# Kernel tuning notes

Measured on AMD Instinct MI355X. Metric: run time of the kernel, lower is better.

The kernel has to match this reference:

```python
import jax, jax.numpy as jnp
import numpy as np

B, C, D, H, W = 2, 96, 32, 64, 64
K = 2            # MRConv stride
EPS = 1e-5
SLOPE = 0.2      # LeakyReLU negative slope used by ViG act_layer('leakyrelu')


def conv1x1(x, w, b):
    # 1x1x1 Conv3d == per-voxel channel GEMM. x: [B,Ci,D,H,W], w: [Co,Ci]
    return jnp.einsum('bcdhw,oc->bodhw', x, w) + b[None, :, None, None, None]


def batchnorm(x, g, b):
    # training-mode BatchNorm3d: stats over (B, D, H, W)
    m = x.mean(axis=(0, 2, 3, 4), keepdims=True)
    v = x.var(axis=(0, 2, 3, 4), keepdims=True)
    return (x - m) * jax.lax.rsqrt(v + EPS) * g[None, :, None, None, None] + b[None, :, None, None, None]


def instnorm(x, g, b):
    # InstanceNorm3d: stats over (D, H, W) per sample/channel
    m = x.mean(axis=(2, 3, 4), keepdims=True)
    v = x.var(axis=(2, 3, 4), keepdims=True)
    return (x - m) * jax.lax.rsqrt(v + EPS) * g[None, :, None, None, None] + b[None, :, None, None, None]


def lrelu(x):
    return jnp.where(x >= 0, x, SLOPE * x)


def mr_aggregate(x):
    # MRConv shift/subtract/max, in closed form.
    # Original: x_j = max over axes a, shifts s in range(K, L_a, K) of (x - roll(x, s, a)), init 0.
    # Since shifts cover ALL nonzero multiples of K mod L_a (L_a % K == 0), the rolled values at a
    # position are exactly the other members of its residue class mod K along that axis, and
    # max(0, x - min_excluding_self) == x - min_including_self.  Hence:
    #   x_j = x - min over axes of (strided residue-class min along that axis).
    def axmin(x, axis):
        L = x.shape[axis]
        shp = list(x.shape)
        grp = shp[:axis] + [L // K, K] + shp[axis + 1:]
        xg = x.reshape(grp)
        m = xg.min(axis=axis, keepdims=True)             # min over same residue class
        return jnp.broadcast_to(m, grp).reshape(shp)
    m = jnp.minimum(jnp.minimum(axmin(x, 2), axmin(x, 3)), axmin(x, 4))
    return x - m


def setup_inputs() -> dict:
    key = jax.random.key(0)
    ks = jax.random.split(key, 8)
    f32 = jnp.float32
    def w(k, co, ci):
        return (jax.random.normal(k, (co, ci), dtype=f32) / np.sqrt(ci)).astype(f32)
    return {
        'x': jax.random.normal(ks[0], (B, C, D, H, W), dtype=f32),
        'w_fc1': w(ks[1], C, C), 'b_fc1': jnp.zeros((C,), f32),
        'g_bn1': jnp.ones((C,), f32), 'be_bn1': jnp.zeros((C,), f32),
        'w_g': w(ks[2], 2 * C, 2 * C), 'b_g': jnp.zeros((2 * C,), f32),
        'g_in': jnp.ones((2 * C,), f32), 'be_in': jnp.zeros((2 * C,), f32),
        'w_fc2': w(ks[3], C, 2 * C), 'b_fc2': jnp.zeros((C,), f32),
        'g_bn2': jnp.ones((C,), f32), 'be_bn2': jnp.zeros((C,), f32),
        'w_f1': w(ks[4], 4 * C, C), 'b_f1': jnp.zeros((4 * C,), f32),
        'g_bnf1': jnp.ones((4 * C,), f32), 'be_bnf1': jnp.zeros((4 * C,), f32),
        'w_f2': w(ks[5], C, 4 * C), 'b_f2': jnp.zeros((C,), f32),
        'g_bnf2': jnp.ones((C,), f32), 'be_bnf2': jnp.zeros((C,), f32),
    }


def reference(x, w_fc1, b_fc1, g_bn1, be_bn1, w_g, b_g, g_in, be_in,
              w_fc2, b_fc2, g_bn2, be_bn2, w_f1, b_f1, g_bnf1, be_bnf1,
              w_f2, b_f2, g_bnf2, be_bnf2):
    # ---- Grapher ----
    shortcut = x
    h = batchnorm(conv1x1(x, w_fc1, b_fc1), g_bn1, be_bn1)          # fc1: Conv+BN
    xj = mr_aggregate(h)                                            # MRConv shift-max agg
    hc = jnp.concatenate([h, xj], axis=1)                           # [B,2C,D,H,W]
    hg = lrelu(instnorm(conv1x1(hc, w_g, b_g), g_in, be_in))        # BasicConv: Conv+IN+LeakyReLU
    h = batchnorm(conv1x1(hg, w_fc2, b_fc2), g_bn2, be_bn2)         # fc2: Conv+BN
    x = h + shortcut
    # ---- FFN ----
    shortcut = x
    h = batchnorm(conv1x1(x, w_f1, b_f1), g_bnf1, be_bnf1)
    h = lrelu(h)
    h = batchnorm(conv1x1(h, w_f2, b_f2), g_bnf2, be_bnf2)
    return h + shortcut
```

## Files before the change

### kernel.cpp

```cpp
#include <hip/hip_runtime.h>
#include <hip/hip_bf16.h>


typedef __hip_bfloat16 bf16;
typedef __attribute__((ext_vector_type(8))) short short8;
typedef __attribute__((ext_vector_type(4))) float f4;
typedef __attribute__((ext_vector_type(4))) unsigned short us4;

#define DEV static __device__ __forceinline__

constexpr int Sq  = 131072;
constexpr int NVq = 262144;

DEV float bu2f(unsigned short u) { return __uint_as_float(((unsigned)u) << 16); }
DEV unsigned short f2bu(float f) {
    unsigned i = __float_as_uint(f);
    unsigned r = i + 0x7FFFu + ((i >> 16) & 1u);
    return (unsigned short)(r >> 16);
}
DEV void glds16(const void* g, void* l) {
    __builtin_amdgcn_global_load_lds(
        (const __attribute__((address_space(1))) unsigned*)g,
        (__attribute__((address_space(3))) unsigned*)l, 16, 0, 0);
}

template<int CIRB, int KP, int CO, int BN, int AMODE, bool PERB>
__global__ __launch_bounds__(256)
void conv_k(const char* __restrict__ A0, const char* __restrict__ A1,
            const char* __restrict__ Wb, const float* __restrict__ bias,
            const float* __restrict__ cfA, const float* __restrict__ cfB,
            bf16* __restrict__ Y, float* __restrict__ part)
{
    constexpr int NSTEP = KP / 64;
    constexpr int NF = BN / 16;
    constexpr int BI = BN / 8;
    __shared__ __align__(16) char smem[16384 + BN * 128];
    char* As = smem;
    char* Bs = smem + 16384;

    const int tid = threadIdx.x;
    const int lane = tid & 63, wid = tid >> 6, l16 = lane & 15, lhi = lane >> 4;
    const int gm = blockIdx.x, gy = blockIdx.y;
    const int v0 = gm * 128;
    const int b = gm >> 10;
    const int n0g = gy * BN;

    f4 acc[2][NF];
#pragma unroll
    for (int nf = 0; nf < NF; ++nf) {
        float bb = bias[n0g + nf * 16 + l16];
        f4 t = {bb, bb, bb, bb};
        acc[0][nf] = t; acc[1][nf] = t;
    }

    for (int s = 0; s < NSTEP; ++s) {
        for (int i = wid; i < BI; i += 4) {
            int o = i * 8 + (lane >> 3);
            glds16(Wb + (size_t)(n0g + o) * (KP * 2) + s * 128 + (((lane & 7) ^ (o & 7)) << 4),
                   Bs + i * 1024);
        }
        if constexpr (AMODE == 0) {
            for (int i = wid; i < 16; i += 4) {
                int r = i * 8 + (lane >> 3);
                glds16(A0 + (size_t)(v0 + r) * CIRB + s * 128 + (((lane & 7) ^ (r & 7)) << 4),
                       As + i * 1024);
            }
        } else {
#pragma unroll
            for (int j = 0; j < 4; ++j) {
                int idx = tid + 256 * j;
                int v = idx >> 3, u = idx & 7;
                int k8 = s * 8 + u;
                short8 hh;
                if constexpr (AMODE == 2) {
                    short8 raw = *(const short8*)(A0 + (size_t)(v0 + v) * CIRB + k8 * 16);
                    int cb = b * KP + k8 * 8;
                    f4 a0 = *(const f4*)(cfA + cb), a1 = *(const f4*)(cfA + cb + 4);
                    f4 d0 = *(const f4*)(cfB + cb), d1 = *(const f4*)(cfB + cb + 4);
#pragma unroll
                    for (int e = 0; e < 4; ++e) {
                        float t0 = fmaf(a0[e], bu2f((unsigned short)raw[e]),     d0[e]);
                        float t1 = fmaf(a1[e], bu2f((unsigned short)raw[e + 4]), d1[e]);
                        t0 = fmaxf(t0, 0.2f * t0);
                        t1 = fmaxf(t1, 0.2f * t1);
                        hh[e] = (short)f2bu(t0); hh[e + 4] = (short)f2bu(t1);
                    }
                } else {
                    if (k8 < 12) {
                        short8 raw = *(const short8*)(A0 + (size_t)(v0 + v) * 192 + k8 * 16);
                        int cb = k8 * 8;
                        f4 a0 = *(const f4*)(cfA + cb), a1 = *(const f4*)(cfA + cb + 4);
                        f4 d0 = *(const f4*)(cfB + cb), d1 = *(const f4*)(cfB + cb + 4);
#pragma unroll
                        for (int e = 0; e < 4; ++e) {
                            hh[e]     = (short)f2bu(fmaf(a0[e], bu2f((unsigned short)raw[e]),     d0[e]));
                            hh[e + 4] = (short)f2bu(fmaf(a1[e], bu2f((unsigned short)raw[e + 4]), d1[e]));
                        }
                    } else {
                        hh = *(const short8*)(A1 + (size_t)(v0 + v) * 192 + (k8 - 12) * 16);
                    }
                }
                *(short8*)(As + v * 128 + ((u ^ (v & 7)) << 4)) = hh;
            }
        }
        __syncthreads();
#pragma unroll
        for (int ks = 0; ks < 2; ++ks) {
            int kg = ks * 4 + lhi;
            short8 av[2];
#pragma unroll
            for (int mf = 0; mf < 2; ++mf) {
                int v = wid * 32 + mf * 16 + l16;
                av[mf] = *(const short8*)(As + v * 128 + ((kg ^ (v & 7)) << 4));
            }
#pragma unroll
            for (int nf = 0; nf < NF; ++nf) {
                int o = nf * 16 + l16;
                short8 bv = *(const short8*)(Bs + o * 128 + ((kg ^ (o & 7)) << 4));
                acc[0][nf] = __builtin_amdgcn_mfma_f32_16x16x32_bf16(av[0], bv, acc[0][nf], 0, 0, 0);
                acc[1][nf] = __builtin_amdgcn_mfma_f32_16x16x32_bf16(av[1], bv, acc[1][nf], 0, 0, 0);
            }
        }
        __syncthreads();
    }

#pragma unroll
    for (int mf = 0; mf < 2; ++mf) {
        int vb = v0 + wid * 32 + mf * 16 + lhi * 4;
#pragma unroll
        for (int nf = 0; nf < NF; ++nf) {
            int n = n0g + nf * 16 + l16;
#pragma unroll
            for (int r = 0; r < 4; ++r) {
                bf16 o; *(unsigned short*)&o = f2bu(acc[mf][nf][r]);
                Y[(size_t)(vb + r) * CO + n] = o;
            }
        }
    }
    float* ps = (float*)smem;
#pragma unroll
    for (int nf = 0; nf < NF; ++nf) {
        float sm = 0.f, sq = 0.f;
#pragma unroll
        for (int mf = 0; mf < 2; ++mf)
#pragma unroll
            for (int r = 0; r < 4; ++r) {
                float v = acc[mf][nf][r];
                sm += v; sq += v * v;
            }
        sm += __shfl_xor(sm, 16); sq += __shfl_xor(sq, 16);
        sm += __shfl_xor(sm, 32); sq += __shfl_xor(sq, 32);
        if (lane < 16) {
            ps[(wid * 2 + 0) * BN + nf * 16 + lane] = sm;
            ps[(wid * 2 + 1) * BN + nf * 16 + lane] = sq;
        }
    }
    __syncthreads();
    if (tid < BN) {
        float sm = ps[0 * BN + tid] + ps[2 * BN + tid] + ps[4 * BN + tid] + ps[6 * BN + tid];
        float sq = ps[1 * BN + tid] + ps[3 * BN + tid] + ps[5 * BN + tid] + ps[7 * BN + tid];
        int slot = PERB ? (b * 32 + (gm & 31)) : (gm & 63);
        float* pb = part + (size_t)(gy * 64 + slot) * 2 * BN;
        atomicAdd(&pb[tid], sm);
        atomicAdd(&pb[BN + tid], sq);
    }
}

__global__ __launch_bounds__(256)
void ffn_stats_k(const char* __restrict__ y2, const char* __restrict__ xT,
                 const float* __restrict__ cfA, const float* __restrict__ cfB,
                 const float* __restrict__ biasf1, const char* __restrict__ Wf1,
                 char* __restrict__ x2, float* __restrict__ part)
{
    __shared__ __align__(16) char smem[32768 + 24576];
    __shared__ float ps[8 * 96];
    char* As = smem;
    char* Bs = smem + 32768;

    const int tid = threadIdx.x;
    const int lane = tid & 63, wid = tid >> 6, l16 = lane & 15, lhi = lane >> 4;
    const int gm = blockIdx.x;
    const int v0 = gm * 128;

#pragma unroll
    for (int j = 0; j < 6; ++j) {
        int slot = tid + 256 * j;
        int v = slot / 12, uc = slot % 12, cb = uc * 8;
        short8 yv = *(const short8*)(y2 + (size_t)(v0 + v) * 192 + uc * 16);
        short8 xv = *(const short8*)(xT + (size_t)(v0 + v) * 192 + uc * 16);
        f4 a0 = *(const f4*)(cfA + cb), a1 = *(const f4*)(cfA + cb + 4);
        f4 d0 = *(const f4*)(cfB + cb), d1 = *(const f4*)(cfB + cb + 4);
        short8 o;
#pragma unroll
        for (int e = 0; e < 4; ++e) {
            float t0 = fmaf(a0[e], bu2f((unsigned short)yv[e]),     d0[e]) + bu2f((unsigned short)xv[e]);
            float t1 = fmaf(a1[e], bu2f((unsigned short)yv[e + 4]), d1[e]) + bu2f((unsigned short)xv[e + 4]);
            o[e]     = (short)f2bu(t0);
            o[e + 4] = (short)f2bu(t1);
        }
        *(short8*)(x2 + (size_t)(v0 + v) * 192 + uc * 16) = o;
        *(short8*)(As + v * 256 + ((uc ^ (v & 7)) << 4)) = o;
    }

    for (int q = 0; q < 4; ++q) {
        for (int i = wid; i < 24; i += 4) {
            int o = i * 4 + (lane >> 4), u = lane & 15;
            glds16(Wf1 + (size_t)(q * 96 + o) * 192 + ((u ^ (o & 7)) << 4),
                   Bs + i * 1024);
        }
        __syncthreads();
        f4 acc[2][6];
#pragma unroll
        for (int nf = 0; nf < 6; ++nf) {
            float bb = biasf1[q * 96 + nf * 16 + l16];
            f4 t = {bb, bb, bb, bb};
            acc[0][nf] = t; acc[1][nf] = t;
        }
#pragma unroll
        for (int ks = 0; ks < 3; ++ks) {
            int kg = ks * 4 + lhi;
            short8 av[2];
#pragma unroll
            for (int mf = 0; mf < 2; ++mf) {
                int v = wid * 32 + mf * 16 + l16;
                av[mf] = *(const short8*)(As + v * 256 + ((kg ^ (v & 7)) << 4));
            }
#pragma unroll
            for (int nf = 0; nf < 6; ++nf) {
                int o = nf * 16 + l16;
                short8 bv = *(const short8*)(Bs + o * 256 + ((kg ^ (o & 7)) << 4));
                acc[0][nf] = __builtin_amdgcn_mfma_f32_16x16x32_bf16(av[0], bv, acc[0][nf], 0, 0, 0);
                acc[1][nf] = __builtin_amdgcn_mfma_f32_16x16x32_bf16(av[1], bv, acc[1][nf], 0, 0, 0);
            }
        }
#pragma unroll
        for (int nf = 0; nf < 6; ++nf) {
            float sm = 0.f, sq = 0.f;
#pragma unroll
            for (int mf = 0; mf < 2; ++mf)
#pragma unroll
                for (int r = 0; r < 4; ++r) {
                    float v = acc[mf][nf][r];
                    sm += v; sq += v * v;
                }
            sm += __shfl_xor(sm, 16); sq += __shfl_xor(sq, 16);
            sm += __shfl_xor(sm, 32); sq += __shfl_xor(sq, 32);
            if (lane < 16) {
                ps[(wid * 2 + 0) * 96 + nf * 16 + lane] = sm;
                ps[(wid * 2 + 1) * 96 + nf * 16 + lane] = sq;
            }
        }
        __syncthreads();
        if (tid < 96) {
            float sm = ps[0 * 96 + tid] + ps[2 * 96 + tid] + ps[4 * 96 + tid] + ps[6 * 96 + tid];
            float sq = ps[1 * 96 + tid] + ps[3 * 96 + tid] + ps[5 * 96 + tid] + ps[7 * 96 + tid];
            float* pb = part + (size_t)(q * 64 + (gm & 63)) * 192;
            atomicAdd(&pb[tid], sm);
            atomicAdd(&pb[96 + tid], sq);
        }
    }
}

__global__ __launch_bounds__(256)
void ffn_k(const char* __restrict__ x2, const float* __restrict__ cfA4,
           const float* __restrict__ cfB4, const float* __restrict__ biasf2,
           const char* __restrict__ Wf1, const char* __restrict__ Wf2,
           bf16* __restrict__ y4, float* __restrict__ part)
{
    __shared__ __align__(16) char smem[32768 + 16384 + 12288 + 16384];
    char* As  = smem;
    char* W1c = smem + 32768;
    char* W2c = smem + 49152;
    char* zb  = smem + 61440;
    float* ps = (float*)zb;

    const int tid = threadIdx.x;
    const int lane = tid & 63, wid = tid >> 6, l16 = lane & 15, lhi = lane >> 4;
    const int gm = blockIdx.x;
    const int v0 = gm * 128;

    for (int i = wid; i < 32; i += 4) {
        int v = i * 4 + (lane >> 4), u = lane & 15;
        glds16(x2 + (size_t)(v0 + v) * 192 + ((u ^ (v & 7)) << 4), As + i * 1024);
    }

    f4 accY[2][6];
#pragma unroll
    for (int nf = 0; nf < 6; ++nf) {
        float bb = biasf2[nf * 16 + l16];
        f4 t = {bb, bb, bb, bb};
        accY[0][nf] = t; accY[1][nf] = t;
    }

    for (int nc = 0; nc < 6; ++nc) {
        for (int i = wid; i < 16; i += 4) {
            int o = i * 4 + (lane >> 4), u = lane & 15;
            glds16(Wf1 + (size_t)(nc * 64 + o) * 192 + ((u ^ (o & 7)) << 4),
                   W1c + i * 1024);
        }
        for (int i = wid; i < 12; i += 4) {
            int o = i * 8 + (lane >> 3), u = lane & 7;
            glds16(Wf2 + (size_t)o * 768 + nc * 128 + ((u ^ (o & 7)) << 4),
                   W2c + i * 1024);
        }
        __syncthreads();
        f4 z[4][2];
#pragma unroll
        for (int mt = 0; mt < 4; ++mt)
#pragma unroll
            for (int nt = 0; nt < 2; ++nt) z[mt][nt] = {0.f, 0.f, 0.f, 0.f};
#pragma unroll
        for (int ks = 0; ks < 3; ++ks) {
            int kg = ks * 4 + lhi;
            short8 xv[2];
#pragma unroll
            for (int nt = 0; nt < 2; ++nt) {
                int v = wid * 32 + nt * 16 + l16;
                xv[nt] = *(const short8*)(As + v * 256 + ((kg ^ (v & 7)) << 4));
            }
#pragma unroll
            for (int mt = 0; mt < 4; ++mt) {
                int o = mt * 16 + l16;
                short8 wv = *(const short8*)(W1c + o * 256 + ((kg ^ (o & 7)) << 4));
                z[mt][0] = __builtin_amdgcn_mfma_f32_16x16x32_bf16(wv, xv[0], z[mt][0], 0, 0, 0);
                z[mt][1] = __builtin_amdgcn_mfma_f32_16x16x32_bf16(wv, xv[1], z[mt][1], 0, 0, 0);
            }
        }
#pragma unroll
        for (int mt = 0; mt < 4; ++mt) {
            int ch = nc * 64 + mt * 16 + lhi * 4;
            f4 a = *(const f4*)(cfA4 + ch);
            f4 bb = *(const f4*)(cfB4 + ch);
#pragma unroll
            for (int nt = 0; nt < 2; ++nt) {
                int v = wid * 32 + nt * 16 + l16;
                us4 p;
#pragma unroll
                for (int r = 0; r < 4; ++r) {
                    float t = fmaf(a[r], z[mt][nt][r], bb[r]);
                    t = fmaxf(t, 0.2f * t);
                    p[r] = f2bu(t);
                }
                *(us4*)(zb + v * 128 + (((mt * 2 + (lhi >> 1)) ^ (v & 7)) << 4) + ((lhi & 1) << 3)) = p;
            }
        }
        __syncthreads();
#pragma unroll
        for (int ks = 0; ks < 2; ++ks) {
            int kg = ks * 4 + lhi;
            short8 av[2];
#pragma unroll
            for (int mf = 0; mf < 2; ++mf) {
                int v = wid * 32 + mf * 16 + l16;
                av[mf] = *(const short8*)(zb + v * 128 + ((kg ^ (v & 7)) << 4));
            }
#pragma unroll
            for (int nf = 0; nf < 6; ++nf) {
                int o = nf * 16 + l16;
                short8 bv = *(const short8*)(W2c + o * 128 + ((kg ^ (o & 7)) << 4));
                accY[0][nf] = __builtin_amdgcn_mfma_f32_16x16x32_bf16(av[0], bv, accY[0][nf], 0, 0, 0);
                accY[1][nf] = __builtin_amdgcn_mfma_f32_16x16x32_bf16(av[1], bv, accY[1][nf], 0, 0, 0);
            }
        }
        __syncthreads();
    }

#pragma unroll
    for (int mf = 0; mf < 2; ++mf) {
        int vb = v0 + wid * 32 + mf * 16 + lhi * 4;
#pragma unroll
        for (int nf = 0; nf < 6; ++nf) {
            int n = nf * 16 + l16;
#pragma unroll
            for (int r = 0; r < 4; ++r) {
                bf16 o; *(unsigned short*)&o = f2bu(accY[mf][nf][r]);
                y4[(size_t)(vb + r) * 96 + n] = o;
            }
        }
    }
#pragma unroll
    for (int nf = 0; nf < 6; ++nf) {
        float sm = 0.f, sq = 0.f;
#pragma unroll
        for (int mf = 0; mf < 2; ++mf)
#pragma unroll
            for (int r = 0; r < 4; ++r) {
                float v = accY[mf][nf][r];
                sm += v; sq += v * v;
            }
        sm += __shfl_xor(sm, 16); sq += __shfl_xor(sq, 16);
        sm += __shfl_xor(sm, 32); sq += __shfl_xor(sq, 32);
        if (lane < 16) {
            ps[(wid * 2 + 0) * 96 + nf * 16 + lane] = sm;
            ps[(wid * 2 + 1) * 96 + nf * 16 + lane] = sq;
        }
    }
    __syncthreads();
    if (tid < 96) {
        float sm = ps[0 * 96 + tid] + ps[2 * 96 + tid] + ps[4 * 96 + tid] + ps[6 * 96 + tid];
        float sq = ps[1 * 96 + tid] + ps[3 * 96 + tid] + ps[5 * 96 + tid] + ps[7 * 96 + tid];
        float* pb = part + (size_t)(gm & 63) * 192;
        atomicAdd(&pb[tid], sm);
        atomicAdd(&pb[96 + tid], sq);
    }
}

__global__ void finalize_k(const float* __restrict__ part, float* __restrict__ cf,
                           const float* __restrict__ g, const float* __restrict__ be,
                           const float* __restrict__ bias,
                           int nStats, int CO, int BN, int perB, float invN)
{
    int s = blockIdx.x * 64 + threadIdx.x;
    if (s >= nStats) return;
    int ch = perB ? (s % CO) : s;
    int bb = perB ? (s / CO) : 0;
    int gy = ch / BN, c = ch - gy * BN;
    int j0 = perB ? bb * 32 : 0, cnt = perB ? 32 : 64;
    float sm = 0.f, sq = 0.f;
    for (int j = 0; j < cnt; ++j) {
        const float* pb = part + (size_t)(gy * 64 + j0 + j) * 2 * BN;
        sm += pb[c]; sq += pb[BN + c];
    }
    float m = sm * invN;
    float var = fmaf(-m, m, sq * invN);
    float A = g[ch] * rsqrtf(var + 1e-5f);
    cf[s] = A;
    float B = fmaf(-m, A, be[ch]);
    if (bias) B = fmaf(A, bias[ch], B);
    cf[1024 + s] = B;
}

__global__ void wprep_k(const float* __restrict__ w0, const float* __restrict__ w1,
                        const float* __restrict__ w2, const float* __restrict__ w3,
                        const float* __restrict__ w4, bf16* __restrict__ Wb)
{
    int i = blockIdx.x * 256 + threadIdx.x;
    if (i >= 141312) return;
    const float* src; int r, KP, CI, off;
    if (i < 12288)       { src = w0; r = i;          KP = 128; CI = 96;  off = 0; }
    else if (i < 49152)  { src = w1; r = i - 12288;  KP = 192; CI = 192; off = 12288; }
    else if (i < 67584)  { src = w2; r = i - 49152;  KP = 192; CI = 192; off = 49152; }
    else if (i < 104448) { src = w3; r = i - 67584;  KP = 96;  CI = 96;  off = 67584; }
    else                 { src = w4; r = i - 104448; KP = 384; CI = 384; off = 104448; }
    int o = r / KP, k = r - o * KP;
    float v = (k < CI) ? src[o * CI + k] : 0.f;
    bf16 h; *(unsigned short*)&h = f2bu(v);
    Wb[off + r] = h;
}

__global__ __launch_bounds__(256)
void tin_k(const float* __restrict__ x, char* __restrict__ xT)
{
    __shared__ float ldsT[128 * 97];
    const int gm = blockIdx.x, b = gm >> 10, s0 = (gm & 1023) * 128;
    const int t = threadIdx.x;
#pragma unroll
    for (int i = 0; i < 12; ++i) {
        int idx = t + 256 * i;
        int c = idx >> 5, s4 = idx & 31;
        f4 r = *(const f4*)(x + ((size_t)(b * 96 + c) << 17) + s0 + s4 * 4);
#pragma unroll
        for (int j = 0; j < 4; ++j) ldsT[(s4 * 4 + j) * 97 + c] = r[j];
    }
    __syncthreads();
#pragma unroll
    for (int i = 0; i < 6; ++i) {
        int idx = t + 256 * i;
        int r = idx / 12, uc = idx % 12, cb = uc * 8;
        short8 o;
#pragma unroll
        for (int e = 0; e < 8; ++e) o[e] = (short)f2bu(ldsT[r * 97 + cb + e]);
        *(short8*)(xT + (size_t)(b * Sq + s0 + r) * 192 + uc * 16) = o;
    }
}

__global__ __launch_bounds__(192)
void mr_dmin_k(const char* __restrict__ y1, char* __restrict__ dminp)
{
    const int wq = blockIdx.x >> 1, dh = blockIdx.x & 1;
    const int h = blockIdx.y, b = blockIdx.z;
    const int t = threadIdx.x;
    const int w = wq * 16 + t / 12, uc = t % 12;
    const char* base = y1 + (size_t)(b * Sq + dh * 16 * 4096 + h * 64 + w) * 192 + uc * 16;
    float mn[2][8];
#pragma unroll
    for (int p = 0; p < 2; ++p)
#pragma unroll
        for (int e = 0; e < 8; ++e) mn[p][e] = 1e30f;
#pragma unroll 4
    for (int i = 0; i < 16; ++i) {
        short8 raw = *(const short8*)(base + (size_t)i * (4096 * 192));
        int p = i & 1;
#pragma unroll
        for (int e = 0; e < 8; ++e)
            mn[p][e] = fminf(mn[p][e], bu2f((unsigned short)raw[e]));
    }
#pragma unroll
    for (int p = 0; p < 2; ++p) {
        short8 o;
#pragma unroll
        for (int e = 0; e < 8; ++e) o[e] = (short)f2bu(mn[p][e]);
        *(short8*)(dminp + (size_t)((((b * 64 + h) * 64 + w) * 2 + dh) * 2 + p) * 192 + uc * 16) = o;
    }
}

__global__ __launch_bounds__(192)
void mr_hmin_k(const char* __restrict__ y1, char* __restrict__ hminp)
{
    const int wq = blockIdx.x >> 2, hq = blockIdx.x & 3;
    const int d = blockIdx.y, b = blockIdx.z;
    const int t = threadIdx.x;
    const int w = wq * 16 + t / 12, uc = t % 12;
    const char* base = y1 + (size_t)(b * Sq + d * 4096 + hq * 16 * 64 + w) * 192 + uc * 16;
    float mn[2][8];
#pragma unroll
    for (int p = 0; p < 2; ++p)
#pragma unroll
        for (int e = 0; e < 8; ++e) mn[p][e] = 1e30f;
#pragma unroll 4
    for (int i = 0; i < 16; ++i) {
        short8 raw = *(const short8*)(base + (size_t)i * (64 * 192));
        int p = i & 1;
#pragma unroll
        for (int e = 0; e < 8; ++e)
            mn[p][e] = fminf(mn[p][e], bu2f((unsigned short)raw[e]));
    }
#pragma unroll
    for (int p = 0; p < 2; ++p) {
        short8 o;
#pragma unroll
        for (int e = 0; e < 8; ++e) o[e] = (short)f2bu(mn[p][e]);
        *(short8*)(hminp + (size_t)((((b * 32 + d) * 64 + w) * 4 + hq) * 2 + p) * 192 + uc * 16) = o;
    }
}

__global__ __launch_bounds__(256)
void mr_p2_k(const char* __restrict__ y1, const float* __restrict__ cfA,
             const char* __restrict__ dminp, const char* __restrict__ hminp,
             char* __restrict__ xj)
{
    __shared__ __align__(16) char rowb[64 * 96 * 2];
    __shared__ float wlds[2 * 96];
    const int h = blockIdx.x, d = blockIdx.y, b = blockIdx.z;
    const int t = threadIdx.x;

    short8 hv[3];
#pragma unroll
    for (int j = 0; j < 3; ++j) {
        int slot = t + 256 * j;
        int w = slot / 12, uc = slot % 12;
        short8 raw = *(const short8*)(y1 + (size_t)(b * Sq + d * 4096 + h * 64 + w) * 192 + uc * 16);
        hv[j] = raw;
        *(short8*)(rowb + slot * 16) = raw;
    }
    __syncthreads();
    if (t < 192) {
        int p = t / 96, c = t % 96;
        float m = 1e30f;
        for (int w2 = p; w2 < 64; w2 += 2)
            m = fminf(m, bu2f(*(const unsigned short*)(rowb + (w2 * 96 + c) * 2)));
        wlds[t] = m;
    }
    __syncthreads();
#pragma unroll
    for (int j = 0; j < 3; ++j) {
        int slot = t + 256 * j;
        int w = slot / 12, uc = slot % 12, cb = uc * 8;
        const char* dp = dminp + (size_t)((((b * 64 + h) * 64 + w) * 2) * 2 + (d & 1)) * 192 + uc * 16;
        short8 dm0 = *(const short8*)(dp);
        short8 dm1 = *(const short8*)(dp + 384);
        const char* hp = hminp + (size_t)((((b * 32 + d) * 64 + w) * 4) * 2 + (h & 1)) * 192 + uc * 16;
        short8 hm0 = *(const short8*)(hp);
        short8 hm1 = *(const short8*)(hp + 384);
        short8 hm2 = *(const short8*)(hp + 768);
        short8 hm3 = *(const short8*)(hp + 1152);
        f4 a0 = *(const f4*)(cfA + cb), a1 = *(const f4*)(cfA + cb + 4);
        short8 xo;
#pragma unroll
        for (int e = 0; e < 8; ++e) {
            float m = fminf(
                fminf(bu2f((unsigned short)dm0[e]), bu2f((unsigned short)dm1[e])),
                fminf(fminf(fminf(bu2f((unsigned short)hm0[e]), bu2f((unsigned short)hm1[e])),
                            fminf(bu2f((unsigned short)hm2[e]), bu2f((unsigned short)hm3[e]))),
                      wlds[(w & 1) * 96 + cb + e]));
            float A = (e < 4) ? a0[e] : a1[e - 4];
            xo[e] = (short)f2bu(A * (bu2f((unsigned short)hv[j][e]) - m));
        }
        *(short8*)(xj + (size_t)(b * Sq + d * 4096 + h * 64 + w) * 192 + uc * 16) = xo;
    }
}

__global__ __launch_bounds__(256)
void tout_k(const char* __restrict__ y4, const float* __restrict__ cfA,
            const float* __restrict__ cfB, const char* __restrict__ x2,
            float* __restrict__ outp)
{
    __shared__ float ldsT[128 * 97];
    const int gm = blockIdx.x, b = gm >> 10, s0 = (gm & 1023) * 128;
    const int t = threadIdx.x;
#pragma unroll
    for (int i = 0; i < 6; ++i) {
        int idx = t + 256 * i;
        int r = idx / 12, uc = idx % 12, cb = uc * 8;
        size_t vv = (size_t)(b * Sq + s0 + r);
        short8 yv = *(const short8*)(y4 + vv * 192 + uc * 16);
        short8 xv = *(const short8*)(x2 + vv * 192 + uc * 16);
        f4 a0 = *(const f4*)(cfA + cb), a1 = *(const f4*)(cfA + cb + 4);
        f4 d0 = *(const f4*)(cfB + cb), d1 = *(const f4*)(cfB + cb + 4);
#pragma unroll
        for (int e = 0; e < 4; ++e) {
            ldsT[r * 97 + cb + e]     = fmaf(a0[e], bu2f((unsigned short)yv[e]),     d0[e]) + bu2f((unsigned short)xv[e]);
            ldsT[r * 97 + cb + e + 4] = fmaf(a1[e], bu2f((unsigned short)yv[e + 4]), d1[e]) + bu2f((unsigned short)xv[e + 4]);
        }
    }
    __syncthreads();
#pragma unroll
    for (int i = 0; i < 12; ++i) {
        int idx = t + 256 * i;
        int c = idx >> 5, s4 = idx & 31;
        f4 o;
#pragma unroll
        for (int j = 0; j < 4; ++j) o[j] = ldsT[(s4 * 4 + j) * 97 + c];
        *(f4*)(outp + ((size_t)(b * 96 + c) << 17) + s0 + s4 * 4) = o;
    }
}

extern "C" void kernel_launch(void* const* d_in, const int* in_sizes, int n_in,
                              void* d_out, int out_size, void* d_ws, size_t ws_size,
                              hipStream_t stream)
{
    (void)in_sizes; (void)n_in; (void)out_size; (void)ws_size;

    const float* x      = (const float*)d_in[0];
    const float* w_fc1  = (const float*)d_in[1];
    const float* b_fc1  = (const float*)d_in[2];
    const float* g_bn1  = (const float*)d_in[3];
    const float* be_bn1 = (const float*)d_in[4];
    const float* w_g    = (const float*)d_in[5];
    const float* b_g    = (const float*)d_in[6];
    const float* g_in   = (const float*)d_in[7];
    const float* be_in  = (const float*)d_in[8];
    const float* w_fc2  = (const float*)d_in[9];
    const float* b_fc2  = (const float*)d_in[10];
    const float* g_bn2  = (const float*)d_in[11];
    const float* be_bn2 = (const float*)d_in[12];
    const float* w_f1   = (const float*)d_in[13];
    const float* b_f1   = (const float*)d_in[14];
    const float* g_bnf1 = (const float*)d_in[15];
    const float* be_bnf1= (const float*)d_in[16];
    const float* w_f2   = (const float*)d_in[17];
    const float* b_f2   = (const float*)d_in[18];
    const float* g_bnf2 = (const float*)d_in[19];
    const float* be_bnf2= (const float*)d_in[20];
    float* outp = (float*)d_out;

    char* W = (char*)d_ws;
    char* xT    = W;
    char* y1    = W + 50331648ull;
    char* dminp = W + 100663296ull;
    char* hminp = W + 113246208ull;
    char* xj    = W + 125829120ull;
    char* yg    = W + 176160768ull;
    char* y2    = W + 50331648ull;
    char* y4    = W + 201326592ull;
    char* x2    = W + 251658240ull;
    char* M     = W + 301989888ull;
    bf16*  Wb   = (bf16*)M;
    float* cf   = (float*)(M + 307200);
    float* part = (float*)(M + 348160);

    hipMemsetAsync(part, 0, 5 * 196608, stream);

    const float invBN = 1.f / (float)NVq, invIN = 1.f / (float)Sq;
    dim3 blk(256);
    float* c1 = cf, *c2 = cf + 2048, *c3 = cf + 4096, *c4 = cf + 6144, *c5 = cf + 8192;
    const char* Wfc1 = (const char*)Wb;
    const char* Wg   = (const char*)Wb + 24576;
    const char* Wfc2 = (const char*)Wb + 98304;
    const char* Wf1  = (const char*)Wb + 135168;
    const char* Wf2  = (const char*)Wb + 208896;

    wprep_k<<<552, blk, 0, stream>>>(w_fc1, w_g, w_fc2, w_f1, w_f2, Wb);
    tin_k<<<2048, blk, 0, stream>>>(x, xT);

    conv_k<192, 128, 96, 96, 0, false><<<dim3(2048, 1), blk, 0, stream>>>(
        xT, nullptr, Wfc1, b_fc1, nullptr, nullptr, (bf16*)y1, part);
    finalize_k<<<2, 64, 0, stream>>>(part, c1, g_bn1, be_bn1, nullptr, 96, 96, 96, 0, invBN);

    mr_dmin_k<<<dim3(8, 64, 2), dim3(192), 0, stream>>>(y1, dminp);
    mr_hmin_k<<<dim3(16, 32, 2), dim3(192), 0, stream>>>(y1, hminp);
    mr_p2_k<<<dim3(64, 32, 2), blk, 0, stream>>>(y1, c1, dminp, hminp, xj);

    conv_k<192, 192, 192, 192, 4, true><<<dim3(2048, 1), blk, 0, stream>>>(
        y1, xj, Wg, b_g, c1, c1 + 1024, (bf16*)yg, part + 49152);
    finalize_k<<<6, 64, 0, stream>>>(part + 49152, c2, g_in, be_in, nullptr, 384, 192, 192, 1, invIN);

    conv_k<384, 192, 96, 96, 2, false><<<dim3(2048, 1), blk, 0, stream>>>(
        yg, nullptr, Wfc2, b_fc2, c2, c2 + 1024, (bf16*)y2, part + 98304);
    finalize_k<<<2, 64, 0, stream>>>(part + 98304, c3, g_bn2, be_bn2, nullptr, 96, 96, 96, 0, invBN);

    ffn_stats_k<<<2048, blk, 0, stream>>>(y2, xT, c3, c3 + 1024, b_f1, Wf1, x2, part + 147456);
    finalize_k<<<6, 64, 0, stream>>>(part + 147456, c4, g_bnf1, be_bnf1, b_f1, 384, 384, 96, 0, invBN);

    ffn_k<<<2048, blk, 0, stream>>>(x2, c4, c4 + 1024, b_f2, Wf1, Wf2, (bf16*)y4, part + 196608);
    finalize_k<<<2, 64, 0, stream>>>(part + 196608, c5, g_bnf2, be_bnf2, nullptr, 96, 96, 96, 0, invBN);

    tout_k<<<2048, blk, 0, stream>>>(y4, c5, c5 + 1024, x2, outp);
}
```

Measured before the change: 451.5 us.

## Use hardware bf16 pack conversion and keep FFN activation fragments in registers

Replaces the software round-to-nearest bf16 conversion with the v_cvt_pk_bf16_f32 instruction across several kernels. The FFN kernels now load their activation fragments straight into registers instead of staging them through LDS. Weight tiles move to an unswizzled k-major LDS layout, and the z buffer is padded to a 144-byte row stride. This cuts LDS footprint (which may raise occupancy) and conversion ALU work, but the new layouts could bring bank conflicts, and in the fused kernel the __syncthreads before reading zb is replaced by a per-wave lgkmcnt wait.

```diff
diff --git a/kernel.cpp b/kernel.cpp
--- a/kernel.cpp
+++ b/kernel.cpp
@@ -5,7 +5,7 @@
 typedef __hip_bfloat16 bf16;
 typedef __attribute__((ext_vector_type(8))) short short8;
 typedef __attribute__((ext_vector_type(4))) float f4;
-typedef __attribute__((ext_vector_type(4))) unsigned short us4;
+typedef __attribute__((ext_vector_type(2))) unsigned uint2v;
 
 #define DEV static __device__ __forceinline__
 
@@ -17,6 +17,17 @@
     unsigned i = __float_as_uint(f);
     unsigned r = i + 0x7FFFu + ((i >> 16) & 1u);
     return (unsigned short)(r >> 16);
+}
+DEV unsigned cvtpk(float a, float b) {
+    unsigned r;
+    asm("v_cvt_pk_bf16_f32 %0, %1, %2" : "=v"(r) : "v"(a), "v"(b));
+    return r;
+}
+DEV short8 pack8(const float* t) {
+    union { unsigned u[4]; short8 s; } r;
+    r.u[0] = cvtpk(t[0], t[1]); r.u[1] = cvtpk(t[2], t[3]);
+    r.u[2] = cvtpk(t[4], t[5]); r.u[3] = cvtpk(t[6], t[7]);
+    return r.s;
 }
 DEV void glds16(const void* g, void* l) {
     __builtin_amdgcn_global_load_lds(
@@ -77,25 +88,28 @@
                     int cb = b * KP + k8 * 8;
                     f4 a0 = *(const f4*)(cfA + cb), a1 = *(const f4*)(cfA + cb + 4);
                     f4 d0 = *(const f4*)(cfB + cb), d1 = *(const f4*)(cfB + cb + 4);
+                    float t[8];
 #pragma unroll
                     for (int e = 0; e < 4; ++e) {
-                        float t0 = fmaf(a0[e], bu2f((unsigned short)raw[e]),     d0[e]);
-                        float t1 = fmaf(a1[e], bu2f((unsigned short)raw[e + 4]), d1[e]);
-                        t0 = fmaxf(t0, 0.2f * t0);
-                        t1 = fmaxf(t1, 0.2f * t1);
-                        hh[e] = (short)f2bu(t0); hh[e + 4] = (short)f2bu(t1);
+                        t[e]     = fmaf(a0[e], bu2f((unsigned short)raw[e]),     d0[e]);
+                        t[e + 4] = fmaf(a1[e], bu2f((unsigned short)raw[e + 4]), d1[e]);
                     }
+#pragma unroll
+                    for (int e = 0; e < 8; ++e) t[e] = fmaxf(t[e], 0.2f * t[e]);
+                    hh = pack8(t);
                 } else {
                     if (k8 < 12) {
                         short8 raw = *(const short8*)(A0 + (size_t)(v0 + v) * 192 + k8 * 16);
                         int cb = k8 * 8;
                         f4 a0 = *(const f4*)(cfA + cb), a1 = *(const f4*)(cfA + cb + 4);
                         f4 d0 = *(const f4*)(cfB + cb), d1 = *(const f4*)(cfB + cb + 4);
+                        float t[8];
 #pragma unroll
                         for (int e = 0; e < 4; ++e) {
-                            hh[e]     = (short)f2bu(fmaf(a0[e], bu2f((unsigned short)raw[e]),     d0[e]));
-                            hh[e + 4] = (short)f2bu(fmaf(a1[e], bu2f((unsigned short)raw[e + 4]), d1[e]));
+                            t[e]     = fmaf(a0[e], bu2f((unsigned short)raw[e]),     d0[e]);
+                            t[e + 4] = fmaf(a1[e], bu2f((unsigned short)raw[e + 4]), d1[e]);
                         }
+                        hh = pack8(t);
                     } else {
                         hh = *(const short8*)(A1 + (size_t)(v0 + v) * 192 + (k8 - 12) * 16);
                     }
@@ -172,41 +186,39 @@
                  const float* __restrict__ biasf1, const char* __restrict__ Wf1,
                  char* __restrict__ x2, float* __restrict__ part)
 {
-    __shared__ __align__(16) char smem[32768 + 24576];
+    __shared__ __align__(16) char Bs[96 * 192];
     __shared__ float ps[8 * 96];
-    char* As = smem;
-    char* Bs = smem + 32768;
 
     const int tid = threadIdx.x;
     const int lane = tid & 63, wid = tid >> 6, l16 = lane & 15, lhi = lane >> 4;
     const int gm = blockIdx.x;
     const int v0 = gm * 128;
 
-#pragma unroll
-    for (int j = 0; j < 6; ++j) {
-        int slot = tid + 256 * j;
-        int v = slot / 12, uc = slot % 12, cb = uc * 8;
-        short8 yv = *(const short8*)(y2 + (size_t)(v0 + v) * 192 + uc * 16);
-        short8 xv = *(const short8*)(xT + (size_t)(v0 + v) * 192 + uc * 16);
-        f4 a0 = *(const f4*)(cfA + cb), a1 = *(const f4*)(cfA + cb + 4);
-        f4 d0 = *(const f4*)(cfB + cb), d1 = *(const f4*)(cfB + cb + 4);
-        short8 o;
-#pragma unroll
-        for (int e = 0; e < 4; ++e) {
-            float t0 = fmaf(a0[e], bu2f((unsigned short)yv[e]),     d0[e]) + bu2f((unsigned short)xv[e]);
-            float t1 = fmaf(a1[e], bu2f((unsigned short)yv[e + 4]), d1[e]) + bu2f((unsigned short)xv[e + 4]);
-            o[e]     = (short)f2bu(t0);
-            o[e + 4] = (short)f2bu(t1);
-        }
-        *(short8*)(x2 + (size_t)(v0 + v) * 192 + uc * 16) = o;
-        *(short8*)(As + v * 256 + ((uc ^ (v & 7)) << 4)) = o;
-    }
+    short8 afr[2][3];
+#pragma unroll
+    for (int mf = 0; mf < 2; ++mf)
+#pragma unroll
+        for (int ks = 0; ks < 3; ++ks) {
+            int v = v0 + wid * 32 + mf * 16 + l16;
+            int kg = ks * 4 + lhi, cb = kg * 8;
+            short8 yv = *(const short8*)(y2 + (size_t)v * 192 + kg * 16);
+            short8 xv = *(const short8*)(xT + (size_t)v * 192 + kg * 16);
+            f4 a0 = *(const f4*)(cfA + cb), a1 = *(const f4*)(cfA + cb + 4);
+            f4 d0 = *(const f4*)(cfB + cb), d1 = *(const f4*)(cfB + cb + 4);
+            float t[8];
+#pragma unroll
+            for (int e = 0; e < 4; ++e) {
+                t[e]     = fmaf(a0[e], bu2f((unsigned short)yv[e]),     d0[e]) + bu2f((unsigned short)xv[e]);
+                t[e + 4] = fmaf(a1[e], bu2f((unsigned short)yv[e + 4]), d1[e]) + bu2f((unsigned short)xv[e + 4]);
+            }
+            afr[mf][ks] = pack8(t);
+            *(short8*)(x2 + (size_t)v * 192 + kg * 16) = afr[mf][ks];
+        }
 
     for (int q = 0; q < 4; ++q) {
-        for (int i = wid; i < 24; i += 4) {
-            int o = i * 4 + (lane >> 4), u = lane & 15;
-            glds16(Wf1 + (size_t)(q * 96 + o) * 192 + ((u ^ (o & 7)) << 4),
-                   Bs + i * 1024);
+        for (int i = tid; i < 1152; i += 256) {
+            int u = i / 96, o = i - u * 96;
+            glds16(Wf1 + (size_t)(q * 96 + o) * 192 + (u << 4), Bs + (size_t)i * 16);
         }
         __syncthreads();
         f4 acc[2][6];
@@ -219,18 +231,12 @@
 #pragma unroll
         for (int ks = 0; ks < 3; ++ks) {
             int kg = ks * 4 + lhi;
-            short8 av[2];
-#pragma unroll
-            for (int mf = 0; mf < 2; ++mf) {
-                int v = wid * 32 + mf * 16 + l16;
-                av[mf] = *(const short8*)(As + v * 256 + ((kg ^ (v & 7)) << 4));
-            }
 #pragma unroll
             for (int nf = 0; nf < 6; ++nf) {
                 int o = nf * 16 + l16;
-                short8 bv = *(const short8*)(Bs + o * 256 + ((kg ^ (o & 7)) << 4));
-                acc[0][nf] = __builtin_amdgcn_mfma_f32_16x16x32_bf16(av[0], bv, acc[0][nf], 0, 0, 0);
-                acc[1][nf] = __builtin_amdgcn_mfma_f32_16x16x32_bf16(av[1], bv, acc[1][nf], 0, 0, 0);
+                short8 bv = *(const short8*)(Bs + ((size_t)kg * 96 + o) * 16);
+                acc[0][nf] = __builtin_amdgcn_mfma_f32_16x16x32_bf16(afr[0][ks], bv, acc[0][nf], 0, 0, 0);
+                acc[1][nf] = __builtin_amdgcn_mfma_f32_16x16x32_bf16(afr[1][ks], bv, acc[1][nf], 0, 0, 0);
             }
         }
 #pragma unroll
@@ -258,6 +264,7 @@
             atomicAdd(&pb[tid], sm);
             atomicAdd(&pb[96 + tid], sq);
         }
+        __syncthreads();
     }
 }
 
@@ -267,22 +274,23 @@
            const char* __restrict__ Wf1, const char* __restrict__ Wf2,
            bf16* __restrict__ y4, float* __restrict__ part)
 {
-    __shared__ __align__(16) char smem[32768 + 16384 + 12288 + 16384];
-    char* As  = smem;
-    char* W1c = smem + 32768;
-    char* W2c = smem + 49152;
-    char* zb  = smem + 61440;
-    float* ps = (float*)zb;
+    __shared__ __align__(16) char W1c[12 * 64 * 16];
+    __shared__ __align__(16) char W2c[8 * 96 * 16];
+    __shared__ __align__(16) char zb[128 * 144];
+    __shared__ float ps[8 * 96];
 
     const int tid = threadIdx.x;
     const int lane = tid & 63, wid = tid >> 6, l16 = lane & 15, lhi = lane >> 4;
     const int gm = blockIdx.x;
     const int v0 = gm * 128;
 
-    for (int i = wid; i < 32; i += 4) {
-        int v = i * 4 + (lane >> 4), u = lane & 15;
-        glds16(x2 + (size_t)(v0 + v) * 192 + ((u ^ (v & 7)) << 4), As + i * 1024);
-    }
+    short8 xfr[2][3];
+#pragma unroll
+    for (int nt = 0; nt < 2; ++nt)
+#pragma unroll
+        for (int ks = 0; ks < 3; ++ks)
+            xfr[nt][ks] = *(const short8*)(x2 + (size_t)(v0 + wid * 32 + nt * 16 + l16) * 192
+                                           + (ks * 4 + lhi) * 16);
 
     f4 accY[2][6];
 #pragma unroll
@@ -293,37 +301,28 @@
     }
 
     for (int nc = 0; nc < 6; ++nc) {
-        for (int i = wid; i < 16; i += 4) {
-            int o = i * 4 + (lane >> 4), u = lane & 15;
-            glds16(Wf1 + (size_t)(nc * 64 + o) * 192 + ((u ^ (o & 7)) << 4),
-                   W1c + i * 1024);
-        }
-        for (int i = wid; i < 12; i += 4) {
-            int o = i * 8 + (lane >> 3), u = lane & 7;
-            glds16(Wf2 + (size_t)o * 768 + nc * 128 + ((u ^ (o & 7)) << 4),
-                   W2c + i * 1024);
+        for (int i = tid; i < 768; i += 256) {
+            int u = i / 64, o = i - u * 64;
+            glds16(Wf1 + (size_t)(nc * 64 + o) * 192 + (u << 4), W1c + (size_t)i * 16);
+        }
+        for (int i = tid; i < 768; i += 256) {
+            int u = i / 96, o = i - u * 96;
+            glds16(Wf2 + (size_t)o * 768 + nc * 128 + (u << 4), W2c + (size_t)i * 16);
         }
         __syncthreads();
+
         f4 z[4][2];
 #pragma unroll
-        for (int mt = 0; mt < 4; ++mt)
-#pragma unroll
-            for (int nt = 0; nt < 2; ++nt) z[mt][nt] = {0.f, 0.f, 0.f, 0.f};
+        for (int mt = 0; mt < 4; ++mt) { z[mt][0] = f4{0,0,0,0}; z[mt][1] = f4{0,0,0,0}; }
 #pragma unroll
         for (int ks = 0; ks < 3; ++ks) {
             int kg = ks * 4 + lhi;
-            short8 xv[2];
-#pragma unroll
-            for (int nt = 0; nt < 2; ++nt) {
-                int v = wid * 32 + nt * 16 + l16;
-                xv[nt] = *(const short8*)(As + v * 256 + ((kg ^ (v & 7)) << 4));
-            }
 #pragma unroll
             for (int mt = 0; mt < 4; ++mt) {
                 int o = mt * 16 + l16;
-                short8 wv = *(const short8*)(W1c + o * 256 + ((kg ^ (o & 7)) << 4));
-                z[mt][0] = __builtin_amdgcn_mfma_f32_16x16x32_bf16(wv, xv[0], z[mt][0], 0, 0, 0);
-                z[mt][1] = __builtin_amdgcn_mfma_f32_16x16x32_bf16(wv, xv[1], z[mt][1], 0, 0, 0);
+                short8 wv = *(const short8*)(W1c + ((size_t)kg * 64 + o) * 16);
+                z[mt][0] = __builtin_amdgcn_mfma_f32_16x16x32_bf16(wv, xfr[0][ks], z[mt][0], 0, 0, 0);
+                z[mt][1] = __builtin_amdgcn_mfma_f32_16x16x32_bf16(wv, xfr[1][ks], z[mt][1], 0, 0, 0);
             }
         }
 #pragma unroll
@@ -334,30 +333,27 @@
 #pragma unroll
             for (int nt = 0; nt < 2; ++nt) {
                 int v = wid * 32 + nt * 16 + l16;
-                us4 p;
-#pragma unroll
-                for (int r = 0; r < 4; ++r) {
-                    float t = fmaf(a[r], z[mt][nt][r], bb[r]);
-                    t = fmaxf(t, 0.2f * t);
-                    p[r] = f2bu(t);
-                }
-                *(us4*)(zb + v * 128 + (((mt * 2 + (lhi >> 1)) ^ (v & 7)) << 4) + ((lhi & 1) << 3)) = p;
-            }
-        }
-        __syncthreads();
+                float t0 = fmaf(a[0], z[mt][nt][0], bb[0]); t0 = fmaxf(t0, 0.2f * t0);
+                float t1 = fmaf(a[1], z[mt][nt][1], bb[1]); t1 = fmaxf(t1, 0.2f * t1);
+                float t2 = fmaf(a[2], z[mt][nt][2], bb[2]); t2 = fmaxf(t2, 0.2f * t2);
+                float t3 = fmaf(a[3], z[mt][nt][3], bb[3]); t3 = fmaxf(t3, 0.2f * t3);
+                uint2v w; w[0] = cvtpk(t0, t1); w[1] = cvtpk(t2, t3);
+                *(uint2v*)(zb + (size_t)v * 144 + mt * 32 + lhi * 8) = w;
+            }
+        }
+        asm volatile("s_waitcnt lgkmcnt(0)" ::: "memory");
+        __builtin_amdgcn_sched_barrier(0);
 #pragma unroll
         for (int ks = 0; ks < 2; ++ks) {
             int kg = ks * 4 + lhi;
             short8 av[2];
 #pragma unroll
-            for (int mf = 0; mf < 2; ++mf) {
-                int v = wid * 32 + mf * 16 + l16;
-                av[mf] = *(const short8*)(zb + v * 128 + ((kg ^ (v & 7)) << 4));
-            }
+            for (int mf = 0; mf < 2; ++mf)
+                av[mf] = *(const short8*)(zb + (size_t)(wid * 32 + mf * 16 + l16) * 144 + kg * 16);
 #pragma unroll
             for (int nf = 0; nf < 6; ++nf) {
                 int o = nf * 16 + l16;
-                short8 bv = *(const short8*)(W2c + o * 128 + ((kg ^ (o & 7)) << 4));
+                short8 bv = *(const short8*)(W2c + ((size_t)kg * 96 + o) * 16);
                 accY[0][nf] = __builtin_amdgcn_mfma_f32_16x16x32_bf16(av[0], bv, accY[0][nf], 0, 0, 0);
                 accY[1][nf] = __builtin_amdgcn_mfma_f32_16x16x32_bf16(av[1], bv, accY[1][nf], 0, 0, 0);
             }
@@ -467,10 +463,11 @@
     for (int i = 0; i < 6; ++i) {
         int idx = t + 256 * i;
         int r = idx / 12, uc = idx % 12, cb = uc * 8;
-        short8 o;
-#pragma unroll
-        for (int e = 0; e < 8; ++e) o[e] = (short)f2bu(ldsT[r * 97 + cb + e]);
-        *(short8*)(xT + (size_t)(b * Sq + s0 + r) * 192 + uc * 16) = o;
+        union { unsigned u[4]; short8 s; } o;
+#pragma unroll
+        for (int e = 0; e < 4; ++e)
+            o.u[e] = cvtpk(ldsT[r * 97 + cb + 2 * e], ldsT[r * 97 + cb + 2 * e + 1]);
+        *(short8*)(xT + (size_t)(b * Sq + s0 + r) * 192 + uc * 16) = o.s;
     }
 }
 
```

New measurement: 492.3 us. 9.0% more time.
